# Optimization experiments

Measured on AMD Instinct MI355X. Metric: run time of the kernel, lower is better.

The kernel has to match this reference:

```python
import jax, jax.numpy as jnp
import numpy as np

B, C, H, W = 8, 128, 64, 64


def setup_inputs() -> dict:
    key = jax.random.key(0)
    ks = jax.random.split(key, 9)
    d = C
    return {
        "x": jax.random.normal(ks[0], (B, C, H, W), dtype=jnp.float32),
        "qw": jax.random.normal(ks[1], (d, d), dtype=jnp.float32),
        "qb": jax.random.normal(ks[2], (d,), dtype=jnp.float32),
        "kw": jax.random.normal(ks[3], (d, d), dtype=jnp.float32),
        "kb": jax.random.normal(ks[4], (d,), dtype=jnp.float32),
        "vw": jax.random.normal(ks[5], (d, d), dtype=jnp.float32),
        "vb": jax.random.normal(ks[6], (d,), dtype=jnp.float32),
        "proj_w": jax.random.normal(ks[7], (d, d), dtype=jnp.float32),
        "proj_b": jax.random.normal(ks[8], (d,), dtype=jnp.float32),
    }


def reference(x, qw, qb, kw, kb, vw, vb, proj_w, proj_b):
    b, c, h, w = x.shape
    n = h * w  # number of spatial tokens
    # permute to channels-last and flatten spatial dims: (b, n, c)
    xt = jnp.transpose(x, (0, 2, 3, 1)).reshape(b, n, c)
    q = xt @ qw + qb
    k = xt @ kw + kb
    v = xt @ vw + vb
    scale = c ** (-0.5)
    # full (n x n) attention over flattened spatial tokens, single head
    attn = jax.nn.softmax(jnp.einsum("bnc,bmc->bnm", q, k) * scale, axis=-1)
    hout = jnp.einsum("bnm,bmc->bnc", attn, v) @ proj_w + proj_b
    out = xt + hout  # residual is on the permuted (channels-last) x, per source
    return out.reshape(b, h, w, c)
```

## Files before the change

kernel.cpp:

```cpp
#include <hip/hip_runtime.h>

#define NB 8
#define CD 128
#define NN 4096
#define KV 64
#define SCALE 0.08838834764831845f
#define L2E 1.44269504088896f
#define QSCALE (SCALE * L2E)

typedef __bf16 bf16x8 __attribute__((ext_vector_type(8)));
typedef float f32x4 __attribute__((ext_vector_type(4)));

__device__ __forceinline__ unsigned swz256(unsigned row, unsigned b) {
  unsigned s = b >> 4, o = b & 15u;
  unsigned sw = (s & 8u) | ((s & 7u) ^ (row & 7u));
  return row * 256u + sw * 16u + o;
}
__device__ __forceinline__ unsigned swz128(unsigned row, unsigned b) {
  unsigned s = b >> 4, o = b & 15u;
  unsigned sw = (s ^ row) & 7u;
  return row * 128u + sw * 16u + o;
}

__device__ __forceinline__ int cvt_pk_bf16(float lo, float hi) {
  int w;
  asm("v_cvt_pk_bf16_f32 %0, %1, %2" : "=v"(w) : "v"(lo), "v"(hi));
  return w;
}

__global__ __launch_bounds__(256, 2) void qkv_kernel(
    const float* __restrict__ x,
    const float* __restrict__ qw, const float* __restrict__ qb,
    const float* __restrict__ kw, const float* __restrict__ kb,
    const float* __restrict__ vw, const float* __restrict__ vb,
    __bf16* __restrict__ Qh, __bf16* __restrict__ Ql,
    __bf16* __restrict__ Kh, __bf16* __restrict__ Kl,
    __bf16* __restrict__ Vt)
{
  __shared__ __align__(16) unsigned char sm[49664];
  const int tid = threadIdx.x;
  const int lane = tid & 63, wv = tid >> 6;
  const int l15 = lane & 15, g = lane >> 4;
  const int b = blockIdx.x & 7;
  const int n0 = (blockIdx.x >> 3) * 64;
  const f32x4 Z4 = {0.f, 0.f, 0.f, 0.f};

  #pragma unroll 4
  for (int i = 0; i < 32; ++i) {
    int e = i * 256 + tid;
    int nl = e & 63, c = e >> 6;
    float f = x[((size_t)(b * CD + c)) * NN + n0 + nl];
    __bf16 h = (__bf16)f;
    __bf16 lo = (__bf16)(f - (float)h);
    unsigned off = swz256((unsigned)nl, (unsigned)(c * 2));
    *(__bf16*)(sm + off) = h;
    *(__bf16*)(sm + 16384 + off) = lo;
  }
  __syncthreads();

  bf16x8 ah[4], al[4];
  #pragma unroll
  for (int kk = 0; kk < 4; ++kk) {
    unsigned off = swz256((unsigned)(wv * 16 + l15), (unsigned)(kk * 64 + g * 16));
    ah[kk] = *(const bf16x8*)(sm + off);
    al[kk] = *(const bf16x8*)(sm + 16384 + off);
  }

  for (int mat = 0; mat < 2; ++mat) {
    const float* gw = mat ? kw : qw;
    const float* gb = mat ? kb : qb;
    __bf16* Oh = mat ? Kh : Qh;
    __bf16* Ol = mat ? Kl : Ql;
    const float sc = mat ? 1.0f : QSCALE;
    for (int qd = 0; qd < 4; ++qd) {
      #pragma unroll 4
      for (int i = 0; i < 16; ++i) {
        int e = i * 256 + tid;
        int dl = e & 31, c = e >> 5;
        float f = gw[c * CD + qd * 32 + dl];
        __bf16 h = (__bf16)f;
        __bf16 lo = (__bf16)(f - (float)h);
        unsigned off = swz256((unsigned)dl, (unsigned)(c * 2));
        *(__bf16*)(sm + 32768 + off) = h;
        *(__bf16*)(sm + 40960 + off) = lo;
      }
      __syncthreads();
      #pragma unroll
      for (int fr = 0; fr < 2; ++fr) {
        f32x4 acc = Z4;
        #pragma unroll
        for (int kk = 0; kk < 4; ++kk) {
          unsigned off = swz256((unsigned)(fr * 16 + l15), (unsigned)(kk * 64 + g * 16));
          bf16x8 bh = *(const bf16x8*)(sm + 32768 + off);
          bf16x8 bl = *(const bf16x8*)(sm + 40960 + off);
          acc = __builtin_amdgcn_mfma_f32_16x16x32_bf16(ah[kk], bh, acc, 0, 0, 0);
          acc = __builtin_amdgcn_mfma_f32_16x16x32_bf16(ah[kk], bl, acc, 0, 0, 0);
          acc = __builtin_amdgcn_mfma_f32_16x16x32_bf16(al[kk], bh, acc, 0, 0, 0);
        }
        const int dout = qd * 32 + fr * 16 + l15;
        const float bias = gb[dout];
        #pragma unroll
        for (int r = 0; r < 4; ++r) {
          int row = n0 + wv * 16 + g * 4 + r;
          float v = (acc[r] + bias) * sc;
          __bf16 h = (__bf16)v;
          __bf16 lo = (__bf16)(v - (float)h);
          size_t go = ((size_t)(b * NN + row)) * CD + dout;
          Oh[go] = h;
          Ol[go] = lo;
        }
      }
      __syncthreads();
    }
  }

  f32x4 accV[8];
  #pragma unroll
  for (int i = 0; i < 8; ++i) accV[i] = Z4;
  for (int qd = 0; qd < 4; ++qd) {
    #pragma unroll 4
    for (int i = 0; i < 16; ++i) {
      int e = i * 256 + tid;
      int dl = e & 31, c = e >> 5;
      float f = vw[c * CD + qd * 32 + dl];
      *(__bf16*)(sm + 32768 + swz256((unsigned)dl, (unsigned)(c * 2))) = (__bf16)f;
    }
    __syncthreads();
    #pragma unroll
    for (int fr = 0; fr < 2; ++fr) {
      f32x4 acc = accV[qd * 2 + fr];
      #pragma unroll
      for (int kk = 0; kk < 4; ++kk) {
        unsigned off = swz256((unsigned)(fr * 16 + l15), (unsigned)(kk * 64 + g * 16));
        bf16x8 bh = *(const bf16x8*)(sm + 32768 + off);
        acc = __builtin_amdgcn_mfma_f32_16x16x32_bf16(ah[kk], bh, acc, 0, 0, 0);
      }
      accV[qd * 2 + fr] = acc;
    }
    __syncthreads();
  }
  #pragma unroll
  for (int df = 0; df < 8; ++df) {
    int dout = df * 16 + l15;
    float bias = vb[dout];
    #pragma unroll
    for (int r = 0; r < 4; ++r) {
      int row = wv * 16 + g * 4 + r;
      *(__bf16*)(sm + 32768 + (row * 132 + dout) * 2) = (__bf16)(accV[df][r] + bias);
    }
  }
  __syncthreads();
  #pragma unroll 4
  for (int i = 0; i < 32; ++i) {
    int e = i * 256 + tid;
    int nl = e & 63, dout = e >> 6;
    __bf16 v = *(const __bf16*)(sm + 32768 + (nl * 132 + dout) * 2);
    Vt[((size_t)(b * CD + dout)) * NN + n0 + nl] = v;
  }
}

__global__ __launch_bounds__(256, 2) void attn_kernel(
    const __bf16* __restrict__ Qh, const __bf16* __restrict__ Ql,
    const __bf16* __restrict__ Kh, const __bf16* __restrict__ Kl,
    const __bf16* __restrict__ Vt, const float* __restrict__ x,
    const float* __restrict__ pw, const float* __restrict__ pb,
    float* __restrict__ out)
{
  __shared__ __align__(16) unsigned char sm[49152];
  const int tid = threadIdx.x;
  const int lane = tid & 63, wv = tid >> 6;
  const int l15 = lane & 15, g = lane >> 4;
  const int b = blockIdx.x & 7;
  const int q0 = (blockIdx.x >> 3) * 64;
  const f32x4 Z4 = {0.f, 0.f, 0.f, 0.f};

  bf16x8 qh[4], ql[4];
  #pragma unroll
  for (int kk = 0; kk < 4; ++kk) {
    size_t off = ((size_t)(b * NN + q0 + wv * 16 + l15)) * CD + kk * 32 + g * 8;
    qh[kk] = *(const bf16x8*)(Qh + off);
    ql[kk] = *(const bf16x8*)(Ql + off);
  }

  bf16x8 bones;
  {
    __bf16 v = (l15 == 0) ? (__bf16)1.0f : (__bf16)0.0f;
    #pragma unroll
    for (int j = 0; j < 8; ++j) bones[j] = v;
  }

  f32x4 accO[8];
  #pragma unroll
  for (int i = 0; i < 8; ++i) accO[i] = Z4;
  f32x4 accL = Z4;
  float mrow = -__builtin_inff();

  bf16x8 pkh[4], pkl[4], pvv[4];
  const int rK = tid >> 4, sK = tid & 15;
  const int rV = tid >> 3, sV = tid & 7;
  const __bf16* bKh = Kh + (size_t)(b * NN) * CD;
  const __bf16* bKl = Kl + (size_t)(b * NN) * CD;
  const __bf16* bVt = Vt + (size_t)(b * CD) * NN;
  int offK[4], offV[4];
  #pragma unroll
  for (int i = 0; i < 4; ++i) {
    offK[i] = (i * 16 + rK) * CD + sK * 8;
    offV[i] = (i * 32 + rV) * NN + sV * 8;
  }
  const int baseAddr = ((g & 1) * 32 + l15) * 4;
  const int addrA = (g * 4) * 4;

  #define ISSUE(KTOFFK, KTOFFV)                                                \
    {                                                                          \
      _Pragma("unroll")                                                        \
      for (int i = 0; i < 4; ++i) {                                            \
        pkh[i] = *(const bf16x8*)(bKh + (KTOFFK) + offK[i]);                   \
        pkl[i] = *(const bf16x8*)(bKl + (KTOFFK) + offK[i]);                   \
        pvv[i] = *(const bf16x8*)(bVt + (KTOFFV) + offV[i]);                   \
      }                                                                        \
    }
  #define COMMIT()                                                             \
    {                                                                          \
      _Pragma("unroll")                                                        \
      for (int i = 0; i < 4; ++i) {                                            \
        unsigned o_ = swz256((unsigned)(i * 16 + rK), (unsigned)(sK * 16));    \
        *(bf16x8*)(sm + o_) = pkh[i];                                          \
        *(bf16x8*)(sm + 16384 + o_) = pkl[i];                                  \
        *(bf16x8*)(sm + 32768 +                                                \
                   swz128((unsigned)(i * 32 + rV), (unsigned)(sV * 16))) = pvv[i]; \
      }                                                                        \
    }

  ISSUE(0, 0);
  COMMIT();
  __syncthreads();

  int ktoffK = KV * CD, ktoffV = KV;
  for (int kt = 0; kt < 64; ++kt) {
    if (kt < 63) ISSUE(ktoffK, ktoffV);
    ktoffK += KV * CD;
    ktoffV += KV;
    __builtin_amdgcn_sched_barrier(0);

    f32x4 s4[4];
    #pragma unroll
    for (int kf = 0; kf < 4; ++kf) s4[kf] = Z4;
    __builtin_amdgcn_s_setprio(1);
    #pragma unroll
    for (int kf = 0; kf < 4; ++kf) {
      #pragma unroll
      for (int kk = 0; kk < 4; ++kk) {
        unsigned off = swz256((unsigned)(kf * 16 + l15), (unsigned)(kk * 64 + g * 16));
        bf16x8 bh = *(const bf16x8*)(sm + off);
        bf16x8 bl = *(const bf16x8*)(sm + 16384 + off);
        s4[kf] = __builtin_amdgcn_mfma_f32_16x16x32_bf16(bh, qh[kk], s4[kf], 0, 0, 0);
        s4[kf] = __builtin_amdgcn_mfma_f32_16x16x32_bf16(bl, qh[kk], s4[kf], 0, 0, 0);
        s4[kf] = __builtin_amdgcn_mfma_f32_16x16x32_bf16(bh, ql[kk], s4[kf], 0, 0, 0);
      }
    }
    __builtin_amdgcn_s_setprio(0);

    float mx = fmaxf(fmaxf(s4[0][0], s4[0][1]), fmaxf(s4[0][2], s4[0][3]));
    #pragma unroll
    for (int kf = 1; kf < 4; ++kf) {
      mx = fmaxf(mx, fmaxf(fmaxf(s4[kf][0], s4[kf][1]),
                           fmaxf(s4[kf][2], s4[kf][3])));
    }
    mx = fmaxf(mx, __shfl_xor(mx, 16));
    mx = fmaxf(mx, __shfl_xor(mx, 32));
    const float mn = fmaxf(mrow, mx);
    const bool grow = mn > mrow;
    #pragma unroll
    for (int kf = 0; kf < 4; ++kf) {
      #pragma unroll
      for (int r = 0; r < 4; ++r) s4[kf][r] = exp2f(s4[kf][r] - mn);
    }
    if (__any((int)grow)) {
      float alpha = exp2f(mrow - mn);
      int aw = __builtin_bit_cast(int, alpha);
      #pragma unroll
      for (int r = 0; r < 4; ++r) {
        float ar = __builtin_bit_cast(float,
                     __builtin_amdgcn_ds_bpermute(addrA + r * 4, aw));
        accL[r] *= ar;
        #pragma unroll
        for (int df = 0; df < 8; ++df) accO[df][r] *= ar;
      }
    }
    mrow = mn;

    int c01[4], c23[4];
    #pragma unroll
    for (int kf = 0; kf < 4; ++kf) {
      c01[kf] = cvt_pk_bf16(s4[kf][0], s4[kf][1]);
      c23[kf] = cvt_pk_bf16(s4[kf][2], s4[kf][3]);
    }
    bf16x8 pa[2];
    #pragma unroll
    for (int kk2 = 0; kk2 < 2; ++kk2) {
      int w[4];
      #pragma unroll
      for (int wi = 0; wi < 4; ++wi) {
        int se = (wi & 1) ? c23[kk2 * 2] : c01[kk2 * 2];
        int so = (wi & 1) ? c23[kk2 * 2 + 1] : c01[kk2 * 2 + 1];
        int a = baseAddr + (wi >> 1) * 64;
        int ve = __builtin_amdgcn_ds_bpermute(a, se);
        int vo = __builtin_amdgcn_ds_bpermute(a, so);
        w[wi] = (g < 2) ? ve : vo;
      }
      int4 wv4 = {w[0], w[1], w[2], w[3]};
      pa[kk2] = __builtin_bit_cast(bf16x8, wv4);
    }

    __builtin_amdgcn_s_setprio(1);
    accL = __builtin_amdgcn_mfma_f32_16x16x32_bf16(pa[0], bones, accL, 0, 0, 0);
    accL = __builtin_amdgcn_mfma_f32_16x16x32_bf16(pa[1], bones, accL, 0, 0, 0);
    #pragma unroll
    for (int df = 0; df < 8; ++df) {
      #pragma unroll
      for (int kk2 = 0; kk2 < 2; ++kk2) {
        bf16x8 bv = *(const bf16x8*)(sm + 32768 +
                      swz128((unsigned)(df * 16 + l15), (unsigned)(kk2 * 64 + g * 16)));
        accO[df] = __builtin_amdgcn_mfma_f32_16x16x32_bf16(pa[kk2], bv, accO[df], 0, 0, 0);
      }
    }
    __builtin_amdgcn_s_setprio(0);

    __syncthreads();
    if (kt < 63) COMMIT();
    __syncthreads();
  }
  #undef ISSUE
  #undef COMMIT

  float rl[4];
  #pragma unroll
  for (int r = 0; r < 4; ++r) {
    float lv = __shfl(accL[r], lane & 48);
    rl[r] = 1.0f / lv;
  }
  #pragma unroll
  for (int df = 0; df < 8; ++df) {
    #pragma unroll
    for (int r = 0; r < 4; ++r) {
      unsigned row = (unsigned)(wv * 16 + g * 4 + r);
      *(__bf16*)(sm + swz256(row, (unsigned)((df * 16 + l15) * 2))) =
          (__bf16)(accO[df][r] * rl[r]);
    }
  }
  #pragma unroll 4
  for (int i = 0; i < 16; ++i) {
    int e = i * 256 + tid;
    int c = e >> 5, d4 = e & 31;
    const float4 w4 = *(const float4*)(pw + c * CD + d4 * 4);
    *(__bf16*)(sm + 16384 + swz256((unsigned)(d4 * 4 + 0), (unsigned)(c * 2))) = (__bf16)w4.x;
    *(__bf16*)(sm + 16384 + swz256((unsigned)(d4 * 4 + 1), (unsigned)(c * 2))) = (__bf16)w4.y;
    *(__bf16*)(sm + 16384 + swz256((unsigned)(d4 * 4 + 2), (unsigned)(c * 2))) = (__bf16)w4.z;
    *(__bf16*)(sm + 16384 + swz256((unsigned)(d4 * 4 + 3), (unsigned)(c * 2))) = (__bf16)w4.w;
  }
  __syncthreads();

  bf16x8 oa[4];
  #pragma unroll
  for (int kk = 0; kk < 4; ++kk)
    oa[kk] = *(const bf16x8*)(sm + swz256((unsigned)(wv * 16 + l15),
                                          (unsigned)(kk * 64 + g * 16)));
  #pragma unroll
  for (int df = 0; df < 8; ++df) {
    f32x4 acc = Z4;
    #pragma unroll
    for (int kk = 0; kk < 4; ++kk) {
      bf16x8 bw = *(const bf16x8*)(sm + 16384 +
                    swz256((unsigned)(df * 16 + l15), (unsigned)(kk * 64 + g * 16)));
      acc = __builtin_amdgcn_mfma_f32_16x16x32_bf16(oa[kk], bw, acc, 0, 0, 0);
    }
    const int cc = df * 16 + l15;
    const float bias = pb[cc];
    #pragma unroll
    for (int r = 0; r < 4; ++r) {
      int row = q0 + wv * 16 + g * 4 + r;
      float val = acc[r] + bias + x[((size_t)(b * CD + cc)) * NN + row];
      out[((size_t)(b * NN + row)) * CD + cc] = val;
    }
  }
}

extern "C" void kernel_launch(void* const* d_in, const int* in_sizes, int n_in,
                              void* d_out, int out_size, void* d_ws, size_t ws_size,
                              hipStream_t stream) {
  (void)in_sizes; (void)n_in; (void)out_size; (void)ws_size;
  const float* x  = (const float*)d_in[0];
  const float* qw = (const float*)d_in[1];
  const float* qb = (const float*)d_in[2];
  const float* kw = (const float*)d_in[3];
  const float* kb = (const float*)d_in[4];
  const float* vw = (const float*)d_in[5];
  const float* vb = (const float*)d_in[6];
  const float* pw = (const float*)d_in[7];
  const float* pb = (const float*)d_in[8];
  float* out = (float*)d_out;

  const size_t SZ = (size_t)NB * NN * CD;
  __bf16* Qh = (__bf16*)d_ws;
  __bf16* Ql = Qh + SZ;
  __bf16* Kh = Ql + SZ;
  __bf16* Kl = Kh + SZ;
  __bf16* Vt = Kl + SZ;

  dim3 grid(512), blk(256);
  qkv_kernel<<<grid, blk, 0, stream>>>(x, qw, qb, kw, kb, vw, vb,
                                       Qh, Ql, Kh, Kl, Vt);
  attn_kernel<<<grid, blk, 0, stream>>>(Qh, Ql, Kh, Kl, Vt, x, pw, pb, out);
}
```

Before: 297.5 us.

## Software-pipeline PV MFMA one tile behind QK with triple-buffered V in LDS

Restructures the attention loop so the P·V product for the previous key tile is issued right after the current tile's QK^T MFMAs, before the softmax of the current tile. This lets matrix work overlap with the exp/max/permute scalar work. V is now held in three LDS buffers (LDS grows from 48KB to 80KB) so the lagged read does not collide with the next commit. The rescale is now applied unconditionally every iteration after the lagged PV. The larger LDS footprint may cut the two-blocks-per-CU occupancy.

```diff
diff --git a/kernel.cpp b/kernel.cpp
--- a/kernel.cpp
+++ b/kernel.cpp
@@ -166,7 +166,7 @@
     const float* __restrict__ pw, const float* __restrict__ pb,
     float* __restrict__ out)
 {
-  __shared__ __align__(16) unsigned char sm[49152];
+  __shared__ __align__(16) unsigned char sm[81920];
   const int tid = threadIdx.x;
   const int lane = tid & 63, wv = tid >> 6;
   const int l15 = lane & 15, g = lane >> 4;
@@ -194,6 +194,10 @@
   for (int i = 0; i < 8; ++i) accO[i] = Z4;
   f32x4 accL = Z4;
   float mrow = -__builtin_inff();
+
+  const int4 zi4 = {0, 0, 0, 0};
+  bf16x8 paA = __builtin_bit_cast(bf16x8, zi4);
+  bf16x8 paB = __builtin_bit_cast(bf16x8, zi4);
 
   bf16x8 pkh[4], pkl[4], pvv[4];
   const int rK = tid >> 4, sK = tid & 15;
@@ -219,23 +223,32 @@
         pvv[i] = *(const bf16x8*)(bVt + (KTOFFV) + offV[i]);                   \
       }                                                                        \
     }
-  #define COMMIT()                                                             \
+  #define COMMIT_K()                                                           \
     {                                                                          \
       _Pragma("unroll")                                                        \
       for (int i = 0; i < 4; ++i) {                                            \
         unsigned o_ = swz256((unsigned)(i * 16 + rK), (unsigned)(sK * 16));    \
         *(bf16x8*)(sm + o_) = pkh[i];                                          \
         *(bf16x8*)(sm + 16384 + o_) = pkl[i];                                  \
-        *(bf16x8*)(sm + 32768 +                                                \
+      }                                                                        \
+    }
+  #define COMMIT_V(VB)                                                         \
+    {                                                                          \
+      _Pragma("unroll")                                                        \
+      for (int i = 0; i < 4; ++i) {                                            \
+        *(bf16x8*)(sm + 32768 + (VB) * 16384 +                                 \
                    swz128((unsigned)(i * 32 + rV), (unsigned)(sV * 16))) = pvv[i]; \
       }                                                                        \
     }
 
   ISSUE(0, 0);
-  COMMIT();
+  COMMIT_K();
+  COMMIT_V(0);
+  COMMIT_V(2);
   __syncthreads();
 
   int ktoffK = KV * CD, ktoffV = KV;
+  int vb_w = 1, vb_r = 2;
   for (int kt = 0; kt < 64; ++kt) {
     if (kt < 63) ISSUE(ktoffK, ktoffV);
     ktoffK += KV * CD;
@@ -260,6 +273,21 @@
     }
     __builtin_amdgcn_s_setprio(0);
 
+    {
+      const unsigned vbase = 32768u + (unsigned)vb_r * 16384u;
+      accL = __builtin_amdgcn_mfma_f32_16x16x32_bf16(paA, bones, accL, 0, 0, 0);
+      accL = __builtin_amdgcn_mfma_f32_16x16x32_bf16(paB, bones, accL, 0, 0, 0);
+      #pragma unroll
+      for (int df = 0; df < 8; ++df) {
+        bf16x8 bv0 = *(const bf16x8*)(sm + vbase +
+                       swz128((unsigned)(df * 16 + l15), (unsigned)(g * 16)));
+        bf16x8 bv1 = *(const bf16x8*)(sm + vbase +
+                       swz128((unsigned)(df * 16 + l15), (unsigned)(64 + g * 16)));
+        accO[df] = __builtin_amdgcn_mfma_f32_16x16x32_bf16(paA, bv0, accO[df], 0, 0, 0);
+        accO[df] = __builtin_amdgcn_mfma_f32_16x16x32_bf16(paB, bv1, accO[df], 0, 0, 0);
+      }
+    }
+
     float mx = fmaxf(fmaxf(s4[0][0], s4[0][1]), fmaxf(s4[0][2], s4[0][3]));
     #pragma unroll
     for (int kf = 1; kf < 4; ++kf) {
@@ -269,25 +297,11 @@
     mx = fmaxf(mx, __shfl_xor(mx, 16));
     mx = fmaxf(mx, __shfl_xor(mx, 32));
     const float mn = fmaxf(mrow, mx);
-    const bool grow = mn > mrow;
     #pragma unroll
     for (int kf = 0; kf < 4; ++kf) {
       #pragma unroll
       for (int r = 0; r < 4; ++r) s4[kf][r] = exp2f(s4[kf][r] - mn);
     }
-    if (__any((int)grow)) {
-      float alpha = exp2f(mrow - mn);
-      int aw = __builtin_bit_cast(int, alpha);
-      #pragma unroll
-      for (int r = 0; r < 4; ++r) {
-        float ar = __builtin_bit_cast(float,
-                     __builtin_amdgcn_ds_bpermute(addrA + r * 4, aw));
-        accL[r] *= ar;
-        #pragma unroll
-        for (int df = 0; df < 8; ++df) accO[df][r] *= ar;
-      }
-    }
-    mrow = mn;
 
     int c01[4], c23[4];
     #pragma unroll
@@ -295,7 +309,7 @@
       c01[kf] = cvt_pk_bf16(s4[kf][0], s4[kf][1]);
       c23[kf] = cvt_pk_bf16(s4[kf][2], s4[kf][3]);
     }
-    bf16x8 pa[2];
+    bf16x8 npa[2];
     #pragma unroll
     for (int kk2 = 0; kk2 < 2; ++kk2) {
       int w[4];
@@ -309,29 +323,50 @@
         w[wi] = (g < 2) ? ve : vo;
       }
       int4 wv4 = {w[0], w[1], w[2], w[3]};
-      pa[kk2] = __builtin_bit_cast(bf16x8, wv4);
-    }
-
-    __builtin_amdgcn_s_setprio(1);
-    accL = __builtin_amdgcn_mfma_f32_16x16x32_bf16(pa[0], bones, accL, 0, 0, 0);
-    accL = __builtin_amdgcn_mfma_f32_16x16x32_bf16(pa[1], bones, accL, 0, 0, 0);
+      npa[kk2] = __builtin_bit_cast(bf16x8, wv4);
+    }
+
+    {
+      float alpha = exp2f(mrow - mn);
+      int aw = __builtin_bit_cast(int, alpha);
+      #pragma unroll
+      for (int r = 0; r < 4; ++r) {
+        float ar = __builtin_bit_cast(float,
+                     __builtin_amdgcn_ds_bpermute(addrA + r * 4, aw));
+        accL[r] *= ar;
+        #pragma unroll
+        for (int df = 0; df < 8; ++df) accO[df][r] *= ar;
+      }
+    }
+    mrow = mn;
+    paA = npa[0];
+    paB = npa[1];
+
+    __syncthreads();
+    if (kt < 63) { COMMIT_K(); COMMIT_V(vb_w); }
+    __syncthreads();
+    vb_w = (vb_w == 2) ? 0 : vb_w + 1;
+    vb_r = (vb_r == 2) ? 0 : vb_r + 1;
+  }
+  #undef ISSUE
+  #undef COMMIT_K
+  #undef COMMIT_V
+
+  {
+    const unsigned vbase = 32768u + (unsigned)vb_r * 16384u;
+    accL = __builtin_amdgcn_mfma_f32_16x16x32_bf16(paA, bones, accL, 0, 0, 0);
+    accL = __builtin_amdgcn_mfma_f32_16x16x32_bf16(paB, bones, accL, 0, 0, 0);
     #pragma unroll
     for (int df = 0; df < 8; ++df) {
-      #pragma unroll
-      for (int kk2 = 0; kk2 < 2; ++kk2) {
-        bf16x8 bv = *(const bf16x8*)(sm + 32768 +
-                      swz128((unsigned)(df * 16 + l15), (unsigned)(kk2 * 64 + g * 16)));
-        accO[df] = __builtin_amdgcn_mfma_f32_16x16x32_bf16(pa[kk2], bv, accO[df], 0, 0, 0);
-      }
-    }
-    __builtin_amdgcn_s_setprio(0);
-
-    __syncthreads();
-    if (kt < 63) COMMIT();
-    __syncthreads();
-  }
-  #undef ISSUE
-  #undef COMMIT
+      bf16x8 bv0 = *(const bf16x8*)(sm + vbase +
+                     swz128((unsigned)(df * 16 + l15), (unsigned)(g * 16)));
+      bf16x8 bv1 = *(const bf16x8*)(sm + vbase +
+                     swz128((unsigned)(df * 16 + l15), (unsigned)(64 + g * 16)));
+      accO[df] = __builtin_amdgcn_mfma_f32_16x16x32_bf16(paA, bv0, accO[df], 0, 0, 0);
+      accO[df] = __builtin_amdgcn_mfma_f32_16x16x32_bf16(paB, bv1, accO[df], 0, 0, 0);
+    }
+  }
+  __syncthreads();
 
   float rl[4];
   #pragma unroll
```

Result: slower. 312.3 us (+5.0%).

## Use two-wave attention blocks with 32 query rows each and async K loads into LDS

Applied to the files above, without the earlier changes.

The attention kernel now runs 128 threads per block, and each wave handles two 16-row query sub-tiles. This lets every K and V fragment read from LDS feed twice as many MFMAs. K hi/lo tiles are double-buffered and loaded straight into LDS with global_load_lds, while V is still staged through registers. The row sum is now computed with shuffles instead of the ones-vector MFMA. The costs are more registers per wave (launch bounds 128,1), 80KB of LDS per block, and fewer waves per CU to hide latency.

```diff
diff --git a/kernel.cpp b/kernel.cpp
--- a/kernel.cpp
+++ b/kernel.cpp
@@ -26,6 +26,12 @@
   int w;
   asm("v_cvt_pk_bf16_f32 %0, %1, %2" : "=v"(w) : "v"(lo), "v"(hi));
   return w;
+}
+
+__device__ __forceinline__ void gload16(const __bf16* g, unsigned char* l) {
+  __builtin_amdgcn_global_load_lds(
+      (const __attribute__((address_space(1))) void*)g,
+      (__attribute__((address_space(3))) void*)l, 16, 0, 0);
 }
 
 __global__ __launch_bounds__(256, 2) void qkv_kernel(
@@ -159,14 +165,14 @@
   }
 }
 
-__global__ __launch_bounds__(256, 2) void attn_kernel(
+__global__ __launch_bounds__(128, 1) void attn_kernel(
     const __bf16* __restrict__ Qh, const __bf16* __restrict__ Ql,
     const __bf16* __restrict__ Kh, const __bf16* __restrict__ Kl,
     const __bf16* __restrict__ Vt, const float* __restrict__ x,
     const float* __restrict__ pw, const float* __restrict__ pb,
     float* __restrict__ out)
 {
-  __shared__ __align__(16) unsigned char sm[49152];
+  __shared__ __align__(16) unsigned char sm[81920];
   const int tid = threadIdx.x;
   const int lane = tid & 63, wv = tid >> 6;
   const int l15 = lane & 15, g = lane >> 4;
@@ -174,183 +180,213 @@
   const int q0 = (blockIdx.x >> 3) * 64;
   const f32x4 Z4 = {0.f, 0.f, 0.f, 0.f};
 
-  bf16x8 qh[4], ql[4];
-  #pragma unroll
-  for (int kk = 0; kk < 4; ++kk) {
-    size_t off = ((size_t)(b * NN + q0 + wv * 16 + l15)) * CD + kk * 32 + g * 8;
-    qh[kk] = *(const bf16x8*)(Qh + off);
-    ql[kk] = *(const bf16x8*)(Ql + off);
-  }
-
-  bf16x8 bones;
-  {
-    __bf16 v = (l15 == 0) ? (__bf16)1.0f : (__bf16)0.0f;
-    #pragma unroll
-    for (int j = 0; j < 8; ++j) bones[j] = v;
-  }
-
-  f32x4 accO[8];
-  #pragma unroll
-  for (int i = 0; i < 8; ++i) accO[i] = Z4;
-  f32x4 accL = Z4;
-  float mrow = -__builtin_inff();
-
-  bf16x8 pkh[4], pkl[4], pvv[4];
-  const int rK = tid >> 4, sK = tid & 15;
-  const int rV = tid >> 3, sV = tid & 7;
+  bf16x8 qh[2][4], ql[2][4];
+  #pragma unroll
+  for (int s = 0; s < 2; ++s) {
+    #pragma unroll
+    for (int kk = 0; kk < 4; ++kk) {
+      size_t off = ((size_t)(b * NN + q0 + wv * 32 + s * 16 + l15)) * CD +
+                   kk * 32 + g * 8;
+      qh[s][kk] = *(const bf16x8*)(Qh + off);
+      ql[s][kk] = *(const bf16x8*)(Ql + off);
+    }
+  }
+
+  f32x4 accO[2][8];
+  #pragma unroll
+  for (int s = 0; s < 2; ++s)
+    #pragma unroll
+    for (int i = 0; i < 8; ++i) accO[s][i] = Z4;
+  float mrow[2] = {-__builtin_inff(), -__builtin_inff()};
+  float lsum[2] = {0.f, 0.f};
+
   const __bf16* bKh = Kh + (size_t)(b * NN) * CD;
   const __bf16* bKl = Kl + (size_t)(b * NN) * CD;
   const __bf16* bVt = Vt + (size_t)(b * CD) * NN;
-  int offK[4], offV[4];
-  #pragma unroll
-  for (int i = 0; i < 4; ++i) {
-    offK[i] = (i * 16 + rK) * CD + sK * 8;
-    offV[i] = (i * 32 + rV) * NN + sV * 8;
-  }
+
+  bf16x8 pvv[8];
+  const int rV = tid >> 3, sV = tid & 7;
+  int offV[8];
+  #pragma unroll
+  for (int i = 0; i < 8; ++i) offV[i] = (i * 16 + rV) * NN + sV * 8;
+
+  const int rKl = lane >> 4, sKd = lane & 15;
+
   const int baseAddr = ((g & 1) * 32 + l15) * 4;
   const int addrA = (g * 4) * 4;
-
-  #define ISSUE(KTOFFK, KTOFFV)                                                \
+  const int addrL = ((lane & 48) * 4);
+
+  #define GLOAD_K(KT, BUF)                                                     \
     {                                                                          \
       _Pragma("unroll")                                                        \
-      for (int i = 0; i < 4; ++i) {                                            \
-        pkh[i] = *(const bf16x8*)(bKh + (KTOFFK) + offK[i]);                   \
-        pkl[i] = *(const bf16x8*)(bKl + (KTOFFK) + offK[i]);                   \
-        pvv[i] = *(const bf16x8*)(bVt + (KTOFFV) + offV[i]);                   \
+      for (int i = 0; i < 8; ++i) {                                            \
+        int r_ = wv * 32 + i * 4 + rKl;                                        \
+        int ss_ = (sKd & 8) | ((sKd & 7) ^ (r_ & 7));                          \
+        size_t goff_ = (size_t)((KT) * KV + r_) * CD + ss_ * 8;                \
+        unsigned lb_ = (unsigned)((BUF) * 16384 + (wv * 32 + i * 4) * 256);    \
+        gload16(bKh + goff_, sm + lb_);                                        \
+        gload16(bKl + goff_, sm + 32768 + lb_);                                \
       }                                                                        \
     }
-  #define COMMIT()                                                             \
+  #define ISSUE_V(KT)                                                          \
     {                                                                          \
       _Pragma("unroll")                                                        \
-      for (int i = 0; i < 4; ++i) {                                            \
-        unsigned o_ = swz256((unsigned)(i * 16 + rK), (unsigned)(sK * 16));    \
-        *(bf16x8*)(sm + o_) = pkh[i];                                          \
-        *(bf16x8*)(sm + 16384 + o_) = pkl[i];                                  \
-        *(bf16x8*)(sm + 32768 +                                                \
-                   swz128((unsigned)(i * 32 + rV), (unsigned)(sV * 16))) = pvv[i]; \
-      }                                                                        \
-    }
-
-  ISSUE(0, 0);
-  COMMIT();
+      for (int i = 0; i < 8; ++i)                                              \
+        pvv[i] = *(const bf16x8*)(bVt + (KT) * KV + offV[i]);                  \
+    }
+  #define COMMIT_V()                                                           \
+    {                                                                          \
+      _Pragma("unroll")                                                        \
+      for (int i = 0; i < 8; ++i)                                              \
+        *(bf16x8*)(sm + 65536 +                                                \
+                   swz128((unsigned)(i * 16 + rV), (unsigned)(sV * 16))) = pvv[i]; \
+    }
+
+  GLOAD_K(0, 0);
+  ISSUE_V(0);
+  COMMIT_V();
   __syncthreads();
 
-  int ktoffK = KV * CD, ktoffV = KV;
   for (int kt = 0; kt < 64; ++kt) {
-    if (kt < 63) ISSUE(ktoffK, ktoffV);
-    ktoffK += KV * CD;
-    ktoffV += KV;
+    const int cur = kt & 1;
+    if (kt < 63) {
+      GLOAD_K(kt + 1, cur ^ 1);
+      ISSUE_V(kt + 1);
+    }
     __builtin_amdgcn_sched_barrier(0);
 
-    f32x4 s4[4];
-    #pragma unroll
-    for (int kf = 0; kf < 4; ++kf) s4[kf] = Z4;
+    f32x4 s4[2][4];
+    #pragma unroll
+    for (int s = 0; s < 2; ++s)
+      #pragma unroll
+      for (int kf = 0; kf < 4; ++kf) s4[s][kf] = Z4;
     __builtin_amdgcn_s_setprio(1);
     #pragma unroll
     for (int kf = 0; kf < 4; ++kf) {
       #pragma unroll
       for (int kk = 0; kk < 4; ++kk) {
-        unsigned off = swz256((unsigned)(kf * 16 + l15), (unsigned)(kk * 64 + g * 16));
+        unsigned off = (unsigned)(cur * 16384) +
+                       swz256((unsigned)(kf * 16 + l15), (unsigned)(kk * 64 + g * 16));
         bf16x8 bh = *(const bf16x8*)(sm + off);
-        bf16x8 bl = *(const bf16x8*)(sm + 16384 + off);
-        s4[kf] = __builtin_amdgcn_mfma_f32_16x16x32_bf16(bh, qh[kk], s4[kf], 0, 0, 0);
-        s4[kf] = __builtin_amdgcn_mfma_f32_16x16x32_bf16(bl, qh[kk], s4[kf], 0, 0, 0);
-        s4[kf] = __builtin_amdgcn_mfma_f32_16x16x32_bf16(bh, ql[kk], s4[kf], 0, 0, 0);
+        bf16x8 bl = *(const bf16x8*)(sm + 32768 + off);
+        #pragma unroll
+        for (int s = 0; s < 2; ++s) {
+          s4[s][kf] = __builtin_amdgcn_mfma_f32_16x16x32_bf16(bh, qh[s][kk], s4[s][kf], 0, 0, 0);
+          s4[s][kf] = __builtin_amdgcn_mfma_f32_16x16x32_bf16(bl, qh[s][kk], s4[s][kf], 0, 0, 0);
+          s4[s][kf] = __builtin_amdgcn_mfma_f32_16x16x32_bf16(bh, ql[s][kk], s4[s][kf], 0, 0, 0);
+        }
       }
     }
     __builtin_amdgcn_s_setprio(0);
 
-    float mx = fmaxf(fmaxf(s4[0][0], s4[0][1]), fmaxf(s4[0][2], s4[0][3]));
-    #pragma unroll
-    for (int kf = 1; kf < 4; ++kf) {
-      mx = fmaxf(mx, fmaxf(fmaxf(s4[kf][0], s4[kf][1]),
-                           fmaxf(s4[kf][2], s4[kf][3])));
-    }
-    mx = fmaxf(mx, __shfl_xor(mx, 16));
-    mx = fmaxf(mx, __shfl_xor(mx, 32));
-    const float mn = fmaxf(mrow, mx);
-    const bool grow = mn > mrow;
-    #pragma unroll
-    for (int kf = 0; kf < 4; ++kf) {
-      #pragma unroll
-      for (int r = 0; r < 4; ++r) s4[kf][r] = exp2f(s4[kf][r] - mn);
-    }
-    if (__any((int)grow)) {
-      float alpha = exp2f(mrow - mn);
+    bf16x8 pa[2][2];
+    #pragma unroll
+    for (int s = 0; s < 2; ++s) {
+      float mx = fmaxf(fmaxf(s4[s][0][0], s4[s][0][1]),
+                       fmaxf(s4[s][0][2], s4[s][0][3]));
+      #pragma unroll
+      for (int kf = 1; kf < 4; ++kf)
+        mx = fmaxf(mx, fmaxf(fmaxf(s4[s][kf][0], s4[s][kf][1]),
+                             fmaxf(s4[s][kf][2], s4[s][kf][3])));
+      mx = fmaxf(mx, __shfl_xor(mx, 16));
+      mx = fmaxf(mx, __shfl_xor(mx, 32));
+      const float mn = fmaxf(mrow[s], mx);
+      float ps = 0.f;
+      #pragma unroll
+      for (int kf = 0; kf < 4; ++kf) {
+        #pragma unroll
+        for (int r = 0; r < 4; ++r) {
+          float p = exp2f(s4[s][kf][r] - mn);
+          s4[s][kf][r] = p;
+          ps += p;
+        }
+      }
+      ps += __shfl_xor(ps, 16);
+      ps += __shfl_xor(ps, 32);
+      const float alpha = exp2f(mrow[s] - mn);
+      lsum[s] = lsum[s] * alpha + ps;
+      mrow[s] = mn;
+
       int aw = __builtin_bit_cast(int, alpha);
       #pragma unroll
       for (int r = 0; r < 4; ++r) {
         float ar = __builtin_bit_cast(float,
                      __builtin_amdgcn_ds_bpermute(addrA + r * 4, aw));
-        accL[r] *= ar;
-        #pragma unroll
-        for (int df = 0; df < 8; ++df) accO[df][r] *= ar;
-      }
-    }
-    mrow = mn;
-
-    int c01[4], c23[4];
-    #pragma unroll
-    for (int kf = 0; kf < 4; ++kf) {
-      c01[kf] = cvt_pk_bf16(s4[kf][0], s4[kf][1]);
-      c23[kf] = cvt_pk_bf16(s4[kf][2], s4[kf][3]);
-    }
-    bf16x8 pa[2];
-    #pragma unroll
-    for (int kk2 = 0; kk2 < 2; ++kk2) {
-      int w[4];
-      #pragma unroll
-      for (int wi = 0; wi < 4; ++wi) {
-        int se = (wi & 1) ? c23[kk2 * 2] : c01[kk2 * 2];
-        int so = (wi & 1) ? c23[kk2 * 2 + 1] : c01[kk2 * 2 + 1];
-        int a = baseAddr + (wi >> 1) * 64;
-        int ve = __builtin_amdgcn_ds_bpermute(a, se);
-        int vo = __builtin_amdgcn_ds_bpermute(a, so);
-        w[wi] = (g < 2) ? ve : vo;
-      }
-      int4 wv4 = {w[0], w[1], w[2], w[3]};
-      pa[kk2] = __builtin_bit_cast(bf16x8, wv4);
+        #pragma unroll
+        for (int df = 0; df < 8; ++df) accO[s][df][r] *= ar;
+      }
+
+      int c01[4], c23[4];
+      #pragma unroll
+      for (int kf = 0; kf < 4; ++kf) {
+        c01[kf] = cvt_pk_bf16(s4[s][kf][0], s4[s][kf][1]);
+        c23[kf] = cvt_pk_bf16(s4[s][kf][2], s4[s][kf][3]);
+      }
+      #pragma unroll
+      for (int kk2 = 0; kk2 < 2; ++kk2) {
+        int w[4];
+        #pragma unroll
+        for (int wi = 0; wi < 4; ++wi) {
+          int se = (wi & 1) ? c23[kk2 * 2] : c01[kk2 * 2];
+          int so = (wi & 1) ? c23[kk2 * 2 + 1] : c01[kk2 * 2 + 1];
+          int a = baseAddr + (wi >> 1) * 64;
+          int ve = __builtin_amdgcn_ds_bpermute(a, se);
+          int vo = __builtin_amdgcn_ds_bpermute(a, so);
+          w[wi] = (g < 2) ? ve : vo;
+        }
+        int4 wv4 = {w[0], w[1], w[2], w[3]};
+        pa[s][kk2] = __builtin_bit_cast(bf16x8, wv4);
+      }
     }
 
     __builtin_amdgcn_s_setprio(1);
-    accL = __builtin_amdgcn_mfma_f32_16x16x32_bf16(pa[0], bones, accL, 0, 0, 0);
-    accL = __builtin_amdgcn_mfma_f32_16x16x32_bf16(pa[1], bones, accL, 0, 0, 0);
     #pragma unroll
     for (int df = 0; df < 8; ++df) {
       #pragma unroll
       for (int kk2 = 0; kk2 < 2; ++kk2) {
-        bf16x8 bv = *(const bf16x8*)(sm + 32768 +
+        bf16x8 bv = *(const bf16x8*)(sm + 65536 +
                       swz128((unsigned)(df * 16 + l15), (unsigned)(kk2 * 64 + g * 16)));
-        accO[df] = __builtin_amdgcn_mfma_f32_16x16x32_bf16(pa[kk2], bv, accO[df], 0, 0, 0);
+        #pragma unroll
+        for (int s = 0; s < 2; ++s)
+          accO[s][df] = __builtin_amdgcn_mfma_f32_16x16x32_bf16(pa[s][kk2], bv, accO[s][df], 0, 0, 0);
       }
     }
     __builtin_amdgcn_s_setprio(0);
 
     __syncthreads();
-    if (kt < 63) COMMIT();
+    if (kt < 63) COMMIT_V();
     __syncthreads();
   }
-  #undef ISSUE
-  #undef COMMIT
-
-  float rl[4];
-  #pragma unroll
-  for (int r = 0; r < 4; ++r) {
-    float lv = __shfl(accL[r], lane & 48);
-    rl[r] = 1.0f / lv;
-  }
-  #pragma unroll
-  for (int df = 0; df < 8; ++df) {
+  #undef GLOAD_K
+  #undef ISSUE_V
+  #undef COMMIT_V
+
+  float rl[2][4];
+  #pragma unroll
+  for (int s = 0; s < 2; ++s) {
+    int lw = __builtin_bit_cast(int, lsum[s]);
     #pragma unroll
     for (int r = 0; r < 4; ++r) {
-      unsigned row = (unsigned)(wv * 16 + g * 4 + r);
-      *(__bf16*)(sm + swz256(row, (unsigned)((df * 16 + l15) * 2))) =
-          (__bf16)(accO[df][r] * rl[r]);
+      float lv = __builtin_bit_cast(float,
+                   __builtin_amdgcn_ds_bpermute(addrL + (g * 4 + r) * 4, lw));
+      rl[s][r] = 1.0f / lv;
+    }
+  }
+  #pragma unroll
+  for (int s = 0; s < 2; ++s) {
+    #pragma unroll
+    for (int df = 0; df < 8; ++df) {
+      #pragma unroll
+      for (int r = 0; r < 4; ++r) {
+        unsigned row = (unsigned)(wv * 32 + s * 16 + g * 4 + r);
+        *(__bf16*)(sm + swz256(row, (unsigned)((df * 16 + l15) * 2))) =
+            (__bf16)(accO[s][df][r] * rl[s][r]);
+      }
     }
   }
   #pragma unroll 4
-  for (int i = 0; i < 16; ++i) {
-    int e = i * 256 + tid;
+  for (int i = 0; i < 32; ++i) {
+    int e = i * 128 + tid;
     int c = e >> 5, d4 = e & 31;
     const float4 w4 = *(const float4*)(pw + c * CD + d4 * 4);
     *(__bf16*)(sm + 16384 + swz256((unsigned)(d4 * 4 + 0), (unsigned)(c * 2))) = (__bf16)w4.x;
@@ -360,27 +396,35 @@
   }
   __syncthreads();
 
-  bf16x8 oa[4];
-  #pragma unroll
-  for (int kk = 0; kk < 4; ++kk)
-    oa[kk] = *(const bf16x8*)(sm + swz256((unsigned)(wv * 16 + l15),
-                                          (unsigned)(kk * 64 + g * 16)));
+  bf16x8 oa[2][4];
+  #pragma unroll
+  for (int s = 0; s < 2; ++s)
+    #pragma unroll
+    for (int kk = 0; kk < 4; ++kk)
+      oa[s][kk] = *(const bf16x8*)(sm +
+                    swz256((unsigned)(wv * 32 + s * 16 + l15),
+                           (unsigned)(kk * 64 + g * 16)));
   #pragma unroll
   for (int df = 0; df < 8; ++df) {
-    f32x4 acc = Z4;
+    f32x4 acc2[2] = {Z4, Z4};
     #pragma unroll
     for (int kk = 0; kk < 4; ++kk) {
       bf16x8 bw = *(const bf16x8*)(sm + 16384 +
                     swz256((unsigned)(df * 16 + l15), (unsigned)(kk * 64 + g * 16)));
-      acc = __builtin_amdgcn_mfma_f32_16x16x32_bf16(oa[kk], bw, acc, 0, 0, 0);
+      #pragma unroll
+      for (int s = 0; s < 2; ++s)
+        acc2[s] = __builtin_amdgcn_mfma_f32_16x16x32_bf16(oa[s][kk], bw, acc2[s], 0, 0, 0);
     }
     const int cc = df * 16 + l15;
     const float bias = pb[cc];
     #pragma unroll
-    for (int r = 0; r < 4; ++r) {
-      int row = q0 + wv * 16 + g * 4 + r;
-      float val = acc[r] + bias + x[((size_t)(b * CD + cc)) * NN + row];
-      out[((size_t)(b * NN + row)) * CD + cc] = val;
+    for (int s = 0; s < 2; ++s) {
+      #pragma unroll
+      for (int r = 0; r < 4; ++r) {
+        int row = q0 + wv * 32 + s * 16 + g * 4 + r;
+        float val = acc2[s][r] + bias + x[((size_t)(b * CD + cc)) * NN + row];
+        out[((size_t)(b * NN + row)) * CD + cc] = val;
+      }
     }
   }
 }
@@ -407,8 +451,8 @@
   __bf16* Kl = Kh + SZ;
   __bf16* Vt = Kl + SZ;
 
-  dim3 grid(512), blk(256);
-  qkv_kernel<<<grid, blk, 0, stream>>>(x, qw, qb, kw, kb, vw, vb,
-                                       Qh, Ql, Kh, Kl, Vt);
-  attn_kernel<<<grid, blk, 0, stream>>>(Qh, Ql, Kh, Kl, Vt, x, pw, pb, out);
-}
+  qkv_kernel<<<dim3(512), dim3(256), 0, stream>>>(x, qw, qb, kw, kb, vw, vb,
+                                                  Qh, Ql, Kh, Kl, Vt);
+  attn_kernel<<<dim3(512), dim3(128), 0, stream>>>(Qh, Ql, Kh, Kl, Vt, x,
+                                                   pw, pb, out);
+}
```

After: 373.7 us. 1.26x slower.
